# Performance work log

Measured on AMD Instinct MI355X. Metric: run time of the kernel, lower is better.

## Reference

```python
import jax, jax.numpy as jnp
import numpy as np
import itertools

RANK = 2  # window size per axis; mode='linear' -> stride 1; rank_op='avg'; rank_mode='drop'


def setup_inputs() -> dict:
    key = jax.random.key(0)
    k1, k2, k3 = jax.random.split(key, 3)
    m = 32
    D = 20
    hypervol = jax.random.normal(k1, (D, D, D, D, m), dtype=jnp.float32)
    # nn.Linear weight init U(-0.5, 0.5); P init U(-0.1, 0.1)
    M_w = jax.random.uniform(k2, (m, m), dtype=jnp.float32, minval=-0.5, maxval=0.5)
    P = jax.random.uniform(k3, (m, m), dtype=jnp.float32, minval=-0.1, maxval=0.1)
    return {"hypervol": hypervol, "M_w": M_w, "P": P}


def reference(hypervol, M_w, P):
    m = P.shape[0]
    D1, D2, D3, D4, _ = hypervol.shape
    o1, o2, o3, o4 = D1 - RANK + 1, D2 - RANK + 1, D3 - RANK + 1, D4 - RANK + 1

    # Vectorized window extraction with mean reduction ('avg'):
    # mean over RANK^4 window = average of RANK^4 shifted slices (fixed small loop).
    acc = jnp.zeros((o1, o2, o3, o4, m), dtype=hypervol.dtype)
    for a, b, c, d in itertools.product(range(RANK), repeat=4):
        acc = acc + hypervol[a:a + o1, b:b + o2, c:c + o3, d:d + o4, :]
    win = acc / float(RANK ** 4)  # [o1,o2,o3,o4,m]

    # M(v): Linear without bias -> v @ W^T
    x = jnp.einsum('abcdj,ij->abcdi', win, M_w)  # [o1,o2,o3,o4,m]
    # note: output index of Linear is i; below x plays role of (M v) with einsum index j
    x = jnp.einsum('abcdi->abcdi', x)  # no-op, keep shape clear

    # periods[i,j] = i*m + j + 2 (identical for all four axes)
    ii = jnp.arange(m, dtype=jnp.float32)
    periods = ii[:, None] * m + ii[None, :] + 2.0  # [m,m]
    two_pi = jnp.float32(2.0 * np.pi)

    def ctab(n):
        k = jnp.arange(n, dtype=jnp.float32)
        return jnp.cos(two_pi * k[:, None, None] / periods)  # [n,m,m]

    C1, C2, C3, C4 = ctab(o1), ctab(o2), ctab(o3), ctab(o4)
    # phi[a,b,c,d,i,j] = C1[a]*C2[b]*C3[c]*C4[d]; built from tiny per-axis tables
    phi = (C1[:, None, None, None] * C2[None, :, None, None]) \
          [:, :, :, None] * 0.0  # placeholder removed below
    phi = (C1[:, None, None, None, :, :]
           * C2[None, :, None, None, :, :]
           * C3[None, None, :, None, :, :]
           * C4[None, None, None, :, :, :])  # [o1,o2,o3,o4,m,m]

    # N(k)_i = sum_j P_ij * (Mv)_j * phi_ij  (matches einsum 'bj,ij,bij->bi')
    Nk = jnp.einsum('abcdj,ij,abcdij->abcdi', x, P, phi)
    return Nk.reshape(-1, m)  # [num_windows, m], window order = k1-major like the loops
```

## Files before the change

### kernel.cpp

```cpp
#include <hip/hip_runtime.h>

#define DD 20
#define MM 32
#define OO 19
#define NWIN (OO*OO*OO)
#define WPB 4
#define NBLK ((NWIN + WPB - 1) / WPB)

#define CS_FLOATS (OO*MM*MM)
#define PS_OFF CS_FLOATS
#define MS_OFF (PS_OFF + MM*MM)
#define WS_FLOATS (MS_OFF + MM*MM)

#define LSLICE 1248
#define WOFF 640

__global__ __launch_bounds__(256) void build_tables_kernel(
        const float* __restrict__ Mw, const float* __restrict__ P,
        float* __restrict__ ws) {
    const int idx = blockIdx.x * 256 + threadIdx.x;
    if (idx < CS_FLOATS) {
        const int k    = idx >> 10;
        const int r    = idx & 1023;
        const int q    = r >> 8;
        const int lane = (r >> 2) & 63;
        const int e    = r & 3;
        const int i    = lane & 31;
        const int j    = (lane >> 5) * 16 + q * 4 + e;
        const float period = (float)(i * MM + j + 2);
        ws[idx] = cosf(6.28318530717958647692f * (float)k / period);
    } else if (idx < WS_FLOATS) {
        const int r    = (idx - PS_OFF) & 1023;
        const int q    = r >> 8;
        const int lane = (r >> 2) & 63;
        const int e    = r & 3;
        const int i    = lane & 31;
        const int j    = (lane >> 5) * 16 + q * 4 + e;
        ws[idx] = (idx < MS_OFF) ? P[i * MM + j]
                                 : Mw[i * MM + j] * 0.0625f;
    }
}

__device__ __forceinline__ void lds_sync() {
    __builtin_amdgcn_s_waitcnt(0xC07F);
    __builtin_amdgcn_wave_barrier();
}

__global__ __launch_bounds__(256, 4) void spatial_kernel(
        const float* __restrict__ H, const float* __restrict__ ws,
        float* __restrict__ out) {
    __shared__ __align__(16) float sLDS[WPB][LSLICE];

    const int tid  = threadIdx.x;
    const int w    = tid >> 6;
    const int lane = tid & 63;
    const int i    = lane & 31;
    const int h    = lane >> 5;
    const int jb   = h * 16;

    const int raw = blockIdx.x;
    const int xcd = raw & 7;
    const int k   = raw >> 3;
    const int sb  = (xcd < 3) ? (xcd * 215 + k) : (645 + (xcd - 3) * 214 + k);
    const int win = sb * WPB + w;
    if (win >= NWIN) return;
    const int c = win % OO;
    const int b = (win / OO) % OO;
    const int a = win / (OO * OO);

    const float4* __restrict__ T = (const float4*)ws;
    float* __restrict__ S = sLDS[w];
    float* __restrict__ W = sLDS[w] + WOFF;
    float* __restrict__ X = sLDS[w];

    float mt[16];
    #pragma unroll
    for (int q = 0; q < 4; ++q) {
        const float4 v = T[(MS_OFF >> 2) + q * 64 + lane];
        mt[q*4+0] = v.x; mt[q*4+1] = v.y; mt[q*4+2] = v.z; mt[q*4+3] = v.w;
    }

    {
        float4 a0 = make_float4(0.f, 0.f, 0.f, 0.f);
        float4 a1 = a0, a2 = a0;
        #pragma unroll
        for (int da = 0; da < 2; ++da)
            #pragma unroll
            for (int db = 0; db < 2; ++db)
                #pragma unroll
                for (int dc = 0; dc < 2; ++dc) {
                    const float4* __restrict__ p = (const float4*)(
                        H + (size_t)((((a + da) * DD + (b + db)) * DD + (c + dc)) * DD) * MM);
                    const float4 v0 = p[lane];
                    const float4 v1 = p[64 + lane];
                    a0.x += v0.x; a0.y += v0.y; a0.z += v0.z; a0.w += v0.w;
                    a1.x += v1.x; a1.y += v1.y; a1.z += v1.z; a1.w += v1.w;
                    if (lane < 32) {
                        const float4 v2 = p[128 + lane];
                        a2.x += v2.x; a2.y += v2.y; a2.z += v2.z; a2.w += v2.w;
                    }
                }
        ((float4*)S)[lane]      = a0;
        ((float4*)S)[64 + lane] = a1;
        if (lane < 32) ((float4*)S)[128 + lane] = a2;
    }
    lds_sync();

    #pragma unroll
    for (int t = 0; t < 10; ++t) {
        const int idx = t * 64 + lane;
        if (idx < OO * MM)
            W[idx] = S[idx] + S[idx + MM];
    }
    lds_sync();

    #pragma unroll
    for (int d = 0; d < OO; ++d) {
        const float4* __restrict__ wr = (const float4*)(W + d * MM + jb);
        float t = 0.f;
        #pragma unroll
        for (int q = 0; q < 4; ++q) {
            const float4 v = wr[q];
            t += v.x * mt[q*4+0] + v.y * mt[q*4+1]
               + v.z * mt[q*4+2] + v.w * mt[q*4+3];
        }
        t += __shfl_xor(t, 32, 64);
        if (h == 0) X[d * MM + i] = t;
    }
    lds_sync();

    float s0[16], s1[16], t2c[16];
    #pragma unroll
    for (int q = 0; q < 4; ++q) {
        const float4 pv = T[(PS_OFF >> 2) + q * 64 + lane];
        const float4 va = T[(a * 4 + q) * 64 + lane];
        const float4 vb = T[(b * 4 + q) * 64 + lane];
        const float4 vc = T[(c * 4 + q) * 64 + lane];
        const float4 c1 = T[(1 * 4 + q) * 64 + lane];
        const float qpx = pv.x * va.x * vb.x * vc.x;
        const float qpy = pv.y * va.y * vb.y * vc.y;
        const float qpz = pv.z * va.z * vb.z * vc.z;
        const float qpw = pv.w * va.w * vb.w * vc.w;
        s1[q*4+0] = qpx; s0[q*4+0] = qpx * c1.x; t2c[q*4+0] = c1.x + c1.x;
        s1[q*4+1] = qpy; s0[q*4+1] = qpy * c1.y; t2c[q*4+1] = c1.y + c1.y;
        s1[q*4+2] = qpz; s0[q*4+2] = qpz * c1.z; t2c[q*4+2] = c1.z + c1.z;
        s1[q*4+3] = qpw; s0[q*4+3] = qpw * c1.w; t2c[q*4+3] = c1.w + c1.w;
    }
    const size_t obase = (size_t)win * (OO * MM);
    #pragma unroll
    for (int d = 0; d < OO; ++d) {
        const float4* __restrict__ xr = (const float4*)(X + d * MM + jb);
        float t = 0.f;
        #pragma unroll
        for (int q = 0; q < 4; ++q) {
            const float4 v = xr[q];
            t += v.x * s1[q*4+0] + v.y * s1[q*4+1]
               + v.z * s1[q*4+2] + v.w * s1[q*4+3];
        }
        #pragma unroll
        for (int jj = 0; jj < 16; ++jj) {
            const float nx = __builtin_fmaf(t2c[jj], s1[jj], -s0[jj]);
            s0[jj] = s1[jj];
            s1[jj] = nx;
        }
        t += __shfl_xor(t, 32, 64);
        if (h == 0) out[obase + d * MM + i] = t;
    }
}

extern "C" void kernel_launch(void* const* d_in, const int* in_sizes, int n_in,
                              void* d_out, int out_size, void* d_ws, size_t ws_size,
                              hipStream_t stream) {
    const float* H  = (const float*)d_in[0];
    const float* Mw = (const float*)d_in[1];
    const float* P  = (const float*)d_in[2];
    float* out = (float*)d_out;
    float* ws  = (float*)d_ws;

    build_tables_kernel<<<WS_FLOATS / 256, 256, 0, stream>>>(Mw, P, ws);
    spatial_kernel<<<NBLK, 256, 0, stream>>>(H, ws, out);
}
```

Before: 94.51 us.

## Remap matvec lanes to quad layout with DPP reductions and fuse d-axis pairing

Changes how the table data is laid out so that each lane holds a 4x4 block over (i,j). Per-lane LDS reads shrink from four float4 loads to one, and the partial products are combined across lanes with quad DPP reductions. The d-axis window sum is folded into the M matvec by applying M to all 20 slices and adding adjacent results, which removes the separate W pass and one LDS barrier. The P/phi table setup moves before the H loads so more loads are in flight, at the cost of extra DPP and select instructions and higher register pressure.

```diff
diff --git a/kernel.cpp b/kernel.cpp
--- a/kernel.cpp
+++ b/kernel.cpp
@@ -13,37 +13,44 @@
 #define WS_FLOATS (MS_OFF + MM*MM)
 
 #define LSLICE 1248
-#define WOFF 640
+#define XOFF 640
 
 __global__ __launch_bounds__(256) void build_tables_kernel(
         const float* __restrict__ Mw, const float* __restrict__ P,
         float* __restrict__ ws) {
     const int idx = blockIdx.x * 256 + threadIdx.x;
+    if (idx >= WS_FLOATS) return;
+    const int r10  = idx & 1023;
+    const int r    = r10 >> 8;
+    const int lane = (r10 >> 2) & 63;
+    const int e    = r10 & 3;
+    const int ii   = (lane & 28) + r;
+    const int jj   = ((lane >> 5) << 4) + (lane & 3) * 4 + e;
     if (idx < CS_FLOATS) {
-        const int k    = idx >> 10;
-        const int r    = idx & 1023;
-        const int q    = r >> 8;
-        const int lane = (r >> 2) & 63;
-        const int e    = r & 3;
-        const int i    = lane & 31;
-        const int j    = (lane >> 5) * 16 + q * 4 + e;
-        const float period = (float)(i * MM + j + 2);
-        ws[idx] = cosf(6.28318530717958647692f * (float)k / period);
-    } else if (idx < WS_FLOATS) {
-        const int r    = (idx - PS_OFF) & 1023;
-        const int q    = r >> 8;
-        const int lane = (r >> 2) & 63;
-        const int e    = r & 3;
-        const int i    = lane & 31;
-        const int j    = (lane >> 5) * 16 + q * 4 + e;
-        ws[idx] = (idx < MS_OFF) ? P[i * MM + j]
-                                 : Mw[i * MM + j] * 0.0625f;
+        const int k = idx >> 10;
+        ws[idx] = cosf(6.28318530717958647692f * (float)k
+                       / (float)(ii * MM + jj + 2));
+    } else if (idx < MS_OFF) {
+        ws[idx] = P[ii * MM + jj];
+    } else {
+        ws[idx] = Mw[ii * MM + jj] * 0.0625f;
     }
 }
 
 __device__ __forceinline__ void lds_sync() {
     __builtin_amdgcn_s_waitcnt(0xC07F);
     __builtin_amdgcn_wave_barrier();
+}
+
+template <int CTRL>
+__device__ __forceinline__ float fdpp(float v) {
+    return __int_as_float(__builtin_amdgcn_update_dpp(
+        0, __float_as_int(v), CTRL, 0xF, 0xF, true));
+}
+__device__ __forceinline__ float quad_sum(float v) {
+    v += fdpp<0xB1>(v);
+    v += fdpp<0x4E>(v);
+    return v;
 }
 
 __global__ __launch_bounds__(256, 4) void spatial_kernel(
@@ -56,7 +63,8 @@
     const int lane = tid & 63;
     const int i    = lane & 31;
     const int h    = lane >> 5;
-    const int jb   = h * 16;
+    const int qd   = lane & 3;
+    const int jb2  = (h << 4) + qd * 4;
 
     const int raw = blockIdx.x;
     const int xcd = raw & 7;
@@ -70,14 +78,25 @@
 
     const float4* __restrict__ T = (const float4*)ws;
     float* __restrict__ S = sLDS[w];
-    float* __restrict__ W = sLDS[w] + WOFF;
-    float* __restrict__ X = sLDS[w];
+    float* __restrict__ X = sLDS[w] + XOFF;
 
-    float mt[16];
+    float4 mt[4], s0[4], s1[4], t2c[4];
     #pragma unroll
-    for (int q = 0; q < 4; ++q) {
-        const float4 v = T[(MS_OFF >> 2) + q * 64 + lane];
-        mt[q*4+0] = v.x; mt[q*4+1] = v.y; mt[q*4+2] = v.z; mt[q*4+3] = v.w;
+    for (int r = 0; r < 4; ++r) {
+        const float4 pv = T[(PS_OFF >> 2) + r * 64 + lane];
+        const float4 va = T[(a * 4 + r) * 64 + lane];
+        const float4 vb = T[(b * 4 + r) * 64 + lane];
+        const float4 vc = T[(c * 4 + r) * 64 + lane];
+        const float4 c1 = T[(1 * 4 + r) * 64 + lane];
+        mt[r] = T[(MS_OFF >> 2) + r * 64 + lane];
+        float4 qp;
+        qp.x = pv.x * va.x * vb.x * vc.x;
+        qp.y = pv.y * va.y * vb.y * vc.y;
+        qp.z = pv.z * va.z * vb.z * vc.z;
+        qp.w = pv.w * va.w * vb.w * vc.w;
+        s1[r] = qp;
+        s0[r] = make_float4(qp.x * c1.x, qp.y * c1.y, qp.z * c1.z, qp.w * c1.w);
+        t2c[r] = make_float4(c1.x + c1.x, c1.y + c1.y, c1.z + c1.z, c1.w + c1.w);
     }
 
     {
@@ -106,63 +125,51 @@
     }
     lds_sync();
 
-    #pragma unroll
-    for (int t = 0; t < 10; ++t) {
-        const int idx = t * 64 + lane;
-        if (idx < OO * MM)
-            W[idx] = S[idx] + S[idx + MM];
+    {
+        float yprev = 0.f;
+        #pragma unroll
+        for (int dp = 0; dp < DD; ++dp) {
+            const float4 sv = *(const float4*)(S + dp * MM + jb2);
+            float p0 = sv.x*mt[0].x + sv.y*mt[0].y + sv.z*mt[0].z + sv.w*mt[0].w;
+            float p1 = sv.x*mt[1].x + sv.y*mt[1].y + sv.z*mt[1].z + sv.w*mt[1].w;
+            float p2 = sv.x*mt[2].x + sv.y*mt[2].y + sv.z*mt[2].z + sv.w*mt[2].w;
+            float p3 = sv.x*mt[3].x + sv.y*mt[3].y + sv.z*mt[3].z + sv.w*mt[3].w;
+            const float q0 = quad_sum(p0), q1 = quad_sum(p1);
+            const float q2 = quad_sum(p2), q3 = quad_sum(p3);
+            const float yv = (qd & 1) ? ((qd & 2) ? q3 : q1)
+                                      : ((qd & 2) ? q2 : q0);
+            if (dp > 0) {
+                float xd = yprev + yv;
+                xd += __shfl_xor(xd, 32, 64);
+                if (h == 0) X[(dp - 1) * MM + i] = xd;
+            }
+            yprev = yv;
+        }
     }
     lds_sync();
 
-    #pragma unroll
-    for (int d = 0; d < OO; ++d) {
-        const float4* __restrict__ wr = (const float4*)(W + d * MM + jb);
-        float t = 0.f;
-        #pragma unroll
-        for (int q = 0; q < 4; ++q) {
-            const float4 v = wr[q];
-            t += v.x * mt[q*4+0] + v.y * mt[q*4+1]
-               + v.z * mt[q*4+2] + v.w * mt[q*4+3];
-        }
-        t += __shfl_xor(t, 32, 64);
-        if (h == 0) X[d * MM + i] = t;
-    }
-    lds_sync();
-
-    float s0[16], s1[16], t2c[16];
-    #pragma unroll
-    for (int q = 0; q < 4; ++q) {
-        const float4 pv = T[(PS_OFF >> 2) + q * 64 + lane];
-        const float4 va = T[(a * 4 + q) * 64 + lane];
-        const float4 vb = T[(b * 4 + q) * 64 + lane];
-        const float4 vc = T[(c * 4 + q) * 64 + lane];
-        const float4 c1 = T[(1 * 4 + q) * 64 + lane];
-        const float qpx = pv.x * va.x * vb.x * vc.x;
-        const float qpy = pv.y * va.y * vb.y * vc.y;
-        const float qpz = pv.z * va.z * vb.z * vc.z;
-        const float qpw = pv.w * va.w * vb.w * vc.w;
-        s1[q*4+0] = qpx; s0[q*4+0] = qpx * c1.x; t2c[q*4+0] = c1.x + c1.x;
-        s1[q*4+1] = qpy; s0[q*4+1] = qpy * c1.y; t2c[q*4+1] = c1.y + c1.y;
-        s1[q*4+2] = qpz; s0[q*4+2] = qpz * c1.z; t2c[q*4+2] = c1.z + c1.z;
-        s1[q*4+3] = qpw; s0[q*4+3] = qpw * c1.w; t2c[q*4+3] = c1.w + c1.w;
-    }
     const size_t obase = (size_t)win * (OO * MM);
     #pragma unroll
     for (int d = 0; d < OO; ++d) {
-        const float4* __restrict__ xr = (const float4*)(X + d * MM + jb);
-        float t = 0.f;
+        const float4 xv = *(const float4*)(X + d * MM + jb2);
+        float p0 = xv.x*s1[0].x + xv.y*s1[0].y + xv.z*s1[0].z + xv.w*s1[0].w;
+        float p1 = xv.x*s1[1].x + xv.y*s1[1].y + xv.z*s1[1].z + xv.w*s1[1].w;
+        float p2 = xv.x*s1[2].x + xv.y*s1[2].y + xv.z*s1[2].z + xv.w*s1[2].w;
+        float p3 = xv.x*s1[3].x + xv.y*s1[3].y + xv.z*s1[3].z + xv.w*s1[3].w;
         #pragma unroll
-        for (int q = 0; q < 4; ++q) {
-            const float4 v = xr[q];
-            t += v.x * s1[q*4+0] + v.y * s1[q*4+1]
-               + v.z * s1[q*4+2] + v.w * s1[q*4+3];
+        for (int r = 0; r < 4; ++r) {
+            float4 ns;
+            ns.x = __builtin_fmaf(t2c[r].x, s1[r].x, -s0[r].x);
+            ns.y = __builtin_fmaf(t2c[r].y, s1[r].y, -s0[r].y);
+            ns.z = __builtin_fmaf(t2c[r].z, s1[r].z, -s0[r].z);
+            ns.w = __builtin_fmaf(t2c[r].w, s1[r].w, -s0[r].w);
+            s0[r] = s1[r];
+            s1[r] = ns;
         }
-        #pragma unroll
-        for (int jj = 0; jj < 16; ++jj) {
-            const float nx = __builtin_fmaf(t2c[jj], s1[jj], -s0[jj]);
-            s0[jj] = s1[jj];
-            s1[jj] = nx;
-        }
+        const float q0 = quad_sum(p0), q1 = quad_sum(p1);
+        const float q2 = quad_sum(p2), q3 = quad_sum(p3);
+        float t = (qd & 1) ? ((qd & 2) ? q3 : q1)
+                           : ((qd & 2) ? q2 : q0);
         t += __shfl_xor(t, 32, 64);
         if (h == 0) out[obase + d * MM + i] = t;
     }
@@ -177,6 +184,6 @@
     float* out = (float*)d_out;
     float* ws  = (float*)d_ws;
 
-    build_tables_kernel<<<WS_FLOATS / 256, 256, 0, stream>>>(Mw, P, ws);
+    build_tables_kernel<<<(WS_FLOATS + 255) / 256, 256, 0, stream>>>(Mw, P, ws);
     spatial_kernel<<<NBLK, 256, 0, stream>>>(H, ws, out);
 }
```

After: 119.2 us. 1.26x slower.

## Fuse d-axis pair sum into matvec, shrink LDS, raise occupancy target

Applied to the files above, without the earlier changes.

The separate LDS pass that summed adjacent d-rows is removed. Instead the Mw matvec runs on all 20 raw rows, and consecutive results are added, which relies on linearity. The LDS slice shrinks from 1248 to 640 floats per wave and launch bounds go from 4 to 6 waves per SIMD. Loops are partially unrolled and a sched_barrier is added to limit register pressure. The cost is 20 matvecs instead of 19 and a less aggressive unroll, which may reduce ILP.

```diff
diff --git a/kernel.cpp b/kernel.cpp
--- a/kernel.cpp
+++ b/kernel.cpp
@@ -12,32 +12,27 @@
 #define MS_OFF (PS_OFF + MM*MM)
 #define WS_FLOATS (MS_OFF + MM*MM)
 
-#define LSLICE 1248
-#define WOFF 640
+#define LSLICE 640
 
 __global__ __launch_bounds__(256) void build_tables_kernel(
         const float* __restrict__ Mw, const float* __restrict__ P,
         float* __restrict__ ws) {
     const int idx = blockIdx.x * 256 + threadIdx.x;
+    if (idx >= WS_FLOATS) return;
+    const int r10  = idx & 1023;
+    const int q    = r10 >> 8;
+    const int lane = (r10 >> 2) & 63;
+    const int e    = r10 & 3;
+    const int i    = lane & 31;
+    const int j    = ((lane >> 5) << 4) + q * 4 + e;
     if (idx < CS_FLOATS) {
-        const int k    = idx >> 10;
-        const int r    = idx & 1023;
-        const int q    = r >> 8;
-        const int lane = (r >> 2) & 63;
-        const int e    = r & 3;
-        const int i    = lane & 31;
-        const int j    = (lane >> 5) * 16 + q * 4 + e;
-        const float period = (float)(i * MM + j + 2);
-        ws[idx] = cosf(6.28318530717958647692f * (float)k / period);
-    } else if (idx < WS_FLOATS) {
-        const int r    = (idx - PS_OFF) & 1023;
-        const int q    = r >> 8;
-        const int lane = (r >> 2) & 63;
-        const int e    = r & 3;
-        const int i    = lane & 31;
-        const int j    = (lane >> 5) * 16 + q * 4 + e;
-        ws[idx] = (idx < MS_OFF) ? P[i * MM + j]
-                                 : Mw[i * MM + j] * 0.0625f;
+        const int k = idx >> 10;
+        ws[idx] = cosf(6.28318530717958647692f * (float)k
+                       / (float)(i * MM + j + 2));
+    } else if (idx < MS_OFF) {
+        ws[idx] = P[i * MM + j];
+    } else {
+        ws[idx] = Mw[i * MM + j] * 0.0625f;
     }
 }
 
@@ -46,7 +41,7 @@
     __builtin_amdgcn_wave_barrier();
 }
 
-__global__ __launch_bounds__(256, 4) void spatial_kernel(
+__global__ __launch_bounds__(256, 6) void spatial_kernel(
         const float* __restrict__ H, const float* __restrict__ ws,
         float* __restrict__ out) {
     __shared__ __align__(16) float sLDS[WPB][LSLICE];
@@ -70,21 +65,13 @@
 
     const float4* __restrict__ T = (const float4*)ws;
     float* __restrict__ S = sLDS[w];
-    float* __restrict__ W = sLDS[w] + WOFF;
     float* __restrict__ X = sLDS[w];
-
-    float mt[16];
-    #pragma unroll
-    for (int q = 0; q < 4; ++q) {
-        const float4 v = T[(MS_OFF >> 2) + q * 64 + lane];
-        mt[q*4+0] = v.x; mt[q*4+1] = v.y; mt[q*4+2] = v.z; mt[q*4+3] = v.w;
-    }
 
     {
         float4 a0 = make_float4(0.f, 0.f, 0.f, 0.f);
         float4 a1 = a0, a2 = a0;
         #pragma unroll
-        for (int da = 0; da < 2; ++da)
+        for (int da = 0; da < 2; ++da) {
             #pragma unroll
             for (int db = 0; db < 2; ++db)
                 #pragma unroll
@@ -100,32 +87,48 @@
                         a2.x += v2.x; a2.y += v2.y; a2.z += v2.z; a2.w += v2.w;
                     }
                 }
+            __builtin_amdgcn_sched_barrier(0);
+        }
         ((float4*)S)[lane]      = a0;
         ((float4*)S)[64 + lane] = a1;
         if (lane < 32) ((float4*)S)[128 + lane] = a2;
     }
     lds_sync();
 
-    #pragma unroll
-    for (int t = 0; t < 10; ++t) {
-        const int idx = t * 64 + lane;
-        if (idx < OO * MM)
-            W[idx] = S[idx] + S[idx + MM];
-    }
-    lds_sync();
-
-    #pragma unroll
-    for (int d = 0; d < OO; ++d) {
-        const float4* __restrict__ wr = (const float4*)(W + d * MM + jb);
-        float t = 0.f;
+    {
+        float mt[16];
         #pragma unroll
         for (int q = 0; q < 4; ++q) {
-            const float4 v = wr[q];
-            t += v.x * mt[q*4+0] + v.y * mt[q*4+1]
-               + v.z * mt[q*4+2] + v.w * mt[q*4+3];
+            const float4 v = T[(MS_OFF >> 2) + q * 64 + lane];
+            mt[q*4+0] = v.x; mt[q*4+1] = v.y; mt[q*4+2] = v.z; mt[q*4+3] = v.w;
         }
-        t += __shfl_xor(t, 32, 64);
-        if (h == 0) X[d * MM + i] = t;
+        float yprev;
+        {
+            const float4* __restrict__ sr = (const float4*)(S + 0 * MM + jb);
+            float t = 0.f;
+            #pragma unroll
+            for (int q = 0; q < 4; ++q) {
+                const float4 v = sr[q];
+                t += v.x * mt[q*4+0] + v.y * mt[q*4+1]
+                   + v.z * mt[q*4+2] + v.w * mt[q*4+3];
+            }
+            yprev = t;
+        }
+        #pragma unroll 4
+        for (int dp = 1; dp < DD; ++dp) {
+            const float4* __restrict__ sr = (const float4*)(S + dp * MM + jb);
+            float t = 0.f;
+            #pragma unroll
+            for (int q = 0; q < 4; ++q) {
+                const float4 v = sr[q];
+                t += v.x * mt[q*4+0] + v.y * mt[q*4+1]
+                   + v.z * mt[q*4+2] + v.w * mt[q*4+3];
+            }
+            float xd = yprev + t;
+            xd += __shfl_xor(xd, 32, 64);
+            if (h == 0) X[(dp - 1) * MM + i] = xd;
+            yprev = t;
+        }
     }
     lds_sync();
 
@@ -147,7 +150,7 @@
         s1[q*4+3] = qpw; s0[q*4+3] = qpw * c1.w; t2c[q*4+3] = c1.w + c1.w;
     }
     const size_t obase = (size_t)win * (OO * MM);
-    #pragma unroll
+    #pragma unroll 4
     for (int d = 0; d < OO; ++d) {
         const float4* __restrict__ xr = (const float4*)(X + d * MM + jb);
         float t = 0.f;
@@ -177,6 +180,6 @@
     float* out = (float*)d_out;
     float* ws  = (float*)d_ws;
 
-    build_tables_kernel<<<WS_FLOATS / 256, 256, 0, stream>>>(Mw, P, ws);
+    build_tables_kernel<<<(WS_FLOATS + 255) / 256, 256, 0, stream>>>(Mw, P, ws);
     spatial_kernel<<<NBLK, 256, 0, stream>>>(H, ws, out);
 }
```

Measured after the change: 96.80 us. 2.4% more time.
